# Performance work log

Hardware: AMD Instinct MI355X
Metric: run time of the kernel (lower is better)

Reference implementation:

```python
import jax, jax.numpy as jnp
import numpy as np

E = 8        # n_routed_experts
TOPK = 2     # num_experts_per_tok


def setup_inputs() -> dict:
    key = jax.random.key(0)
    k0, k1, k2, k3, k4 = jax.random.split(key, 5)
    B, S, D, H = 1, 2048, 1024, 2816
    scale = 0.02
    x = jax.random.normal(k0, (B, S, D), jnp.float32)
    Wg = jax.random.normal(k1, (E, D), jnp.float32) * scale   # gate weight [E, D]
    W1 = jax.random.normal(k2, (E, H, D), jnp.float32) * scale  # up-gate proj
    W2 = jax.random.normal(k3, (E, D, H), jnp.float32) * scale  # down proj
    W3 = jax.random.normal(k4, (E, H, D), jnp.float32) * scale  # up proj
    return {"x": x, "Wg": Wg, "W1": W1, "W2": W2, "W3": W3}


def _moe_forward(x, Wg, W1, W2, W3):
    B, S, D = x.shape
    xt = x.reshape(-1, D)                      # [T, D], T = B*S
    T = xt.shape[0]
    # --- gate: logits -> softmax -> top-k, normalized top-k weights ---
    logits = xt @ Wg.T                         # [T, E]
    scores = jax.nn.softmax(logits, axis=-1)
    w, idx = jax.lax.top_k(scores, TOPK)       # [T, K]
    w = w / (w.sum(axis=-1, keepdims=True) + 1e-20)
    # combine weights per token per expert (scatter top-k weights) [T, E]
    cw = jnp.zeros((T, E), xt.dtype).at[jnp.arange(T)[:, None], idx].add(w)
    # --- per-expert SwiGLU FFN (batched over experts) ---
    h = jax.nn.silu(jnp.einsum('td,ehd->teh', xt, W1)) * jnp.einsum('td,ehd->teh', xt, W3)  # [T,E,H]
    out = jnp.einsum('teh,edh->ted', h, W2)    # [T, E, D]
    # weighted combine of selected experts (cw is zero for unselected)
    y = jnp.einsum('te,ted->td', cw, out)      # [T, D]
    return y.reshape(B, S, D)


def reference(x, Wg, W1, W2, W3):
    return _moe_forward(x, Wg, W1, W2, W3)
```

## Files before the change

### kernel.cpp

```cpp
#include <hip/hip_runtime.h>
#include <hip/hip_bf16.h>

#define T_TOK 2048
#define D_DIM 1024
#define H_DIM 2816
#define E_NUM 8
#define CAP   1024

typedef __attribute__((ext_vector_type(8))) short short8;
typedef __attribute__((ext_vector_type(4))) float floatx4;

__device__ __forceinline__ unsigned short f2bf(float f) {
    unsigned int b = __float_as_uint(f);
    b += 0x7FFFu + ((b >> 16) & 1u);
    return (unsigned short)(b >> 16);
}

__device__ __forceinline__ unsigned pk2(float lo, float hi) {
    unsigned a = __float_as_uint(lo) + 0x8000u;
    unsigned b = __float_as_uint(hi) + 0x8000u;
    return __builtin_amdgcn_perm(b, a, 0x07060302);
}

__device__ __forceinline__ short8 pack8r(float4 a, float4 b) {
    union { uint4 u; short8 s; } r;
    r.u.x = pk2(a.x, a.y);
    r.u.y = pk2(a.z, a.w);
    r.u.z = pk2(b.x, b.y);
    r.u.w = pk2(b.z, b.w);
    return r.s;
}

__device__ __forceinline__ void gl2lds16(const void* g, void* l) {
    __builtin_amdgcn_global_load_lds(
        (const __attribute__((address_space(1))) unsigned int*)g,
        (__attribute__((address_space(3))) unsigned int*)l,
        16, 0, 0);
}


__global__ __launch_bounds__(256) void k_gate2(const float* __restrict__ x,
                                               const float* __restrict__ Wg,
                                               int* __restrict__ stok,
                                               float* __restrict__ sw,
                                               int* __restrict__ counts,
                                               unsigned short* __restrict__ xg) {
    const int wave = threadIdx.x >> 6, lane = threadIdx.x & 63;
    const int t = blockIdx.x * 4 + wave;
    const float* xr = x + (size_t)t * D_DIM;
    float acc[E_NUM];
#pragma unroll
    for (int e = 0; e < E_NUM; ++e) acc[e] = 0.f;
#pragma unroll 4
    for (int i = 0; i < D_DIM / 64; ++i) {
        float xv = xr[lane + 64 * i];
#pragma unroll
        for (int e = 0; e < E_NUM; ++e) acc[e] += xv * Wg[e * D_DIM + lane + 64 * i];
    }
#pragma unroll
    for (int e = 0; e < E_NUM; ++e) {
#pragma unroll
        for (int s = 32; s > 0; s >>= 1) acc[e] += __shfl_xor(acc[e], s, 64);
    }
    int slot0 = 0, slot1 = 0;
    if (lane == 0) {
        float mx = acc[0];
#pragma unroll
        for (int e = 1; e < E_NUM; ++e) mx = fmaxf(mx, acc[e]);
        float p[E_NUM], s = 0.f;
#pragma unroll
        for (int e = 0; e < E_NUM; ++e) { p[e] = __expf(acc[e] - mx); s += p[e]; }
        int i0 = 0;
#pragma unroll
        for (int e = 1; e < E_NUM; ++e) if (p[e] > p[i0]) i0 = e;
        int i1 = (i0 == 0) ? 1 : 0;
#pragma unroll
        for (int e = 0; e < E_NUM; ++e) if (e != i0 && p[e] > p[i1]) i1 = e;
        float s0 = p[i0] / s, s1 = p[i1] / s;
        float d = s0 + s1 + 1e-20f;
        int p0 = atomicAdd(&counts[i0], 1); if (p0 >= CAP) p0 = CAP - 1;
        int p1 = atomicAdd(&counts[i1], 1); if (p1 >= CAP) p1 = CAP - 1;
        slot0 = i0 * CAP + p0;
        slot1 = i1 * CAP + p1;
        stok[slot0] = t; sw[slot0] = s0 / d;
        stok[slot1] = t; sw[slot1] = s1 / d;
    }
    slot0 = __shfl(slot0, 0, 64);
    slot1 = __shfl(slot1, 0, 64);
    const float4* xr4 = (const float4*)xr;
    ushort4* xg4 = (ushort4*)xg;
#pragma unroll
    for (int it = 0; it < 4; ++it) {
        float4 v = xr4[lane + 64 * it];
        ushort4 o;
        o.x = f2bf(v.x); o.y = f2bf(v.y); o.z = f2bf(v.z); o.w = f2bf(v.w);
        xg4[(size_t)slot0 * 256 + lane + 64 * it] = o;
        xg4[(size_t)slot1 * 256 + lane + 64 * it] = o;
    }
}

__device__ __forceinline__ void g13_tile(const unsigned char* Ab, const unsigned char* B1b,
                                         const unsigned char* B3b, int agrp, int c0, int c1,
                                         int f8, int f7,
                                         floatx4 (&acc1)[4][2], floatx4 (&acc3)[4][2]) {
    short8 b1f[2][2], b3f[2][2];
#pragma unroll
    for (int n = 0; n < 2; ++n) {
        const int bg = (n * 2 + f8) * 1024 + f7 * 128;
        b1f[n][0] = *(const short8*)(B1b + bg + c0);
        b1f[n][1] = *(const short8*)(B1b + bg + c1);
        b3f[n][0] = *(const short8*)(B3b + bg + c0);
        b3f[n][1] = *(const short8*)(B3b + bg + c1);
    }
#pragma unroll
    for (int m = 0; m < 4; ++m) {
        const unsigned char* ab = Ab + agrp + m * 2048;
        short8 a0 = *(const short8*)(ab + c0);
        short8 a1 = *(const short8*)(ab + c1);
#pragma unroll
        for (int n = 0; n < 2; ++n) {
            acc1[m][n] = __builtin_amdgcn_mfma_f32_16x16x32_bf16(a0, b1f[n][0], acc1[m][n], 0, 0, 0);
            acc1[m][n] = __builtin_amdgcn_mfma_f32_16x16x32_bf16(a1, b1f[n][1], acc1[m][n], 0, 0, 0);
            acc3[m][n] = __builtin_amdgcn_mfma_f32_16x16x32_bf16(a0, b3f[n][0], acc3[m][n], 0, 0, 0);
            acc3[m][n] = __builtin_amdgcn_mfma_f32_16x16x32_bf16(a1, b3f[n][1], acc3[m][n], 0, 0, 0);
        }
    }
}

__global__ __launch_bounds__(256, 2) void k_gemm13(const unsigned short* __restrict__ xg,
                                                   const float* __restrict__ W1,
                                                   const float* __restrict__ W3,
                                                   const int* __restrict__ counts,
                                                   unsigned short* __restrict__ U) {
    const int nt = blockIdx.x;
    const int mt = blockIdx.y;
    const int e  = blockIdx.z;
    const int cnt = min(counts[e], CAP);
    if (mt * 256 >= cnt) return;

    __shared__ __align__(16) unsigned char As[2][32768];
    __shared__ __align__(16) unsigned char B1s[2][4096];
    __shared__ __align__(16) unsigned char B3s[2][4096];

    const int tid = threadIdx.x, lane = tid & 63, wave = tid >> 6;
    const int fr = lane & 15, quad = lane >> 4, f7 = fr & 7, f8 = fr >> 3;

    const unsigned short* aBase = xg
        + ((size_t)e * CAP + mt * 256 + wave * 64 + (lane >> 3)) * D_DIM
        + ((lane & 7) ^ (lane >> 3)) * 8;

    const int br = tid >> 3, bc = tid & 7;
    const float* w1p = W1 + ((size_t)e * H_DIM + nt * 32 + br) * D_DIM + bc * 8;
    const float* w3p = W3 + ((size_t)e * H_DIM + nt * 32 + br) * D_DIM + bc * 8;
    const int bslot = (br >> 3) * 1024 + (br & 7) * 128 + ((bc ^ (br & 7)) << 4);

    floatx4 acc1[4][2], acc3[4][2];
#pragma unroll
    for (int m = 0; m < 4; ++m)
#pragma unroll
        for (int n = 0; n < 2; ++n) { acc1[m][n] = (floatx4)0.f; acc3[m][n] = (floatx4)0.f; }

    const int agrp = (wave * 8 + f8) * 1024 + f7 * 128;
    const int c0 = (quad ^ f7) << 4;
    const int c1 = ((4 | quad) ^ f7) << 4;

#pragma unroll
    for (int j = 0; j < 8; ++j)
        gl2lds16(aBase + (size_t)j * 8 * D_DIM, As[0] + (wave * 8 + j) * 1024);
    {
        float4 u0 = *(const float4*)(w1p);
        float4 u1 = *(const float4*)(w1p + 4);
        float4 v0 = *(const float4*)(w3p);
        float4 v1 = *(const float4*)(w3p + 4);
        *(short8*)(B1s[0] + bslot) = pack8r(u0, u1);
        *(short8*)(B3s[0] + bslot) = pack8r(v0, v1);
    }
    __syncthreads();

    int cur = 0;
#pragma unroll 1
    for (int t = 0; t < D_DIM / 64 - 1; ++t) {
        const int kn = (t + 1) * 64;
#pragma unroll
        for (int j = 0; j < 8; ++j)
            gl2lds16(aBase + (size_t)j * 8 * D_DIM + kn, As[cur ^ 1] + (wave * 8 + j) * 1024);
        float4 u0 = *(const float4*)(w1p + kn);
        float4 u1 = *(const float4*)(w1p + kn + 4);
        float4 v0 = *(const float4*)(w3p + kn);
        float4 v1 = *(const float4*)(w3p + kn + 4);

        g13_tile(As[cur], B1s[cur], B3s[cur], agrp, c0, c1, f8, f7, acc1, acc3);

        *(short8*)(B1s[cur ^ 1] + bslot) = pack8r(u0, u1);
        *(short8*)(B3s[cur ^ 1] + bslot) = pack8r(v0, v1);
        __syncthreads();
        cur ^= 1;
    }
    g13_tile(As[cur], B1s[cur], B3s[cur], agrp, c0, c1, f8, f7, acc1, acc3);

#pragma unroll
    for (int m = 0; m < 4; ++m) {
#pragma unroll
        for (int r = 0; r < 4; ++r) {
            int g = mt * 256 + wave * 64 + m * 16 + quad * 4 + r;
            if (g < cnt) {
                size_t rowb = ((size_t)e * CAP + g) * H_DIM + nt * 32;
#pragma unroll
                for (int n = 0; n < 2; ++n) {
                    float u1v = acc1[m][n][r], u3v = acc3[m][n][r];
                    float u = u1v / (1.f + __expf(-u1v)) * u3v;
                    U[rowb + n * 16 + fr] = f2bf(u);
                }
            }
        }
    }
}

__device__ __forceinline__ void g2_tile(const unsigned char* Ab, const unsigned char* Bb,
                                        int agrp, int c0, int c1, int f8, int f7,
                                        floatx4 (&acc)[4][4]) {
    short8 bf[4][2];
#pragma unroll
    for (int n = 0; n < 4; ++n) {
        const int bg = (n * 2 + f8) * 1024 + f7 * 128;
        bf[n][0] = *(const short8*)(Bb + bg + c0);
        bf[n][1] = *(const short8*)(Bb + bg + c1);
    }
#pragma unroll
    for (int m = 0; m < 4; ++m) {
        const unsigned char* ab = Ab + agrp + m * 2048;
        short8 a0 = *(const short8*)(ab + c0);
        short8 a1 = *(const short8*)(ab + c1);
#pragma unroll
        for (int n = 0; n < 4; ++n) {
            acc[m][n] = __builtin_amdgcn_mfma_f32_16x16x32_bf16(a0, bf[n][0], acc[m][n], 0, 0, 0);
            acc[m][n] = __builtin_amdgcn_mfma_f32_16x16x32_bf16(a1, bf[n][1], acc[m][n], 0, 0, 0);
        }
    }
}

__global__ __launch_bounds__(256, 2) void k_gemm2(const unsigned short* __restrict__ U,
                                                  const float* __restrict__ W2,
                                                  const int* __restrict__ counts,
                                                  const int* __restrict__ stok,
                                                  const float* __restrict__ sw,
                                                  float* __restrict__ y) {
    const int nt = blockIdx.x;
    const int mt = blockIdx.y;
    const int e  = blockIdx.z;
    const int cnt = min(counts[e], CAP);
    if (mt * 256 >= cnt) return;

    __shared__ __align__(16) unsigned char As[2][32768];
    __shared__ __align__(16) unsigned char Bs[2][8192];

    const int tid = threadIdx.x, lane = tid & 63, wave = tid >> 6;
    const int fr = lane & 15, quad = lane >> 4, f7 = fr & 7, f8 = fr >> 3;

    const unsigned short* aBase = U
        + ((size_t)e * CAP + mt * 256 + wave * 64 + (lane >> 3)) * H_DIM
        + ((lane & 7) ^ (lane >> 3)) * 8;

    const int br = tid >> 3, bc = tid & 7;
    const float* w2p0 = W2 + ((size_t)e * D_DIM + nt * 64 + br) * H_DIM + bc * 8;
    const float* w2p1 = w2p0 + (size_t)32 * H_DIM;
    const int bslot0 = (br >> 3) * 1024 + (br & 7) * 128 + ((bc ^ (br & 7)) << 4);
    const int bslot1 = bslot0 + 4096;

    floatx4 acc[4][4];
#pragma unroll
    for (int m = 0; m < 4; ++m)
#pragma unroll
        for (int n = 0; n < 4; ++n) acc[m][n] = (floatx4)0.f;

    const int agrp = (wave * 8 + f8) * 1024 + f7 * 128;
    const int c0 = (quad ^ f7) << 4;
    const int c1 = ((4 | quad) ^ f7) << 4;

#pragma unroll
    for (int j = 0; j < 8; ++j)
        gl2lds16(aBase + (size_t)j * 8 * H_DIM, As[0] + (wave * 8 + j) * 1024);
    {
        float4 u0 = *(const float4*)(w2p0);
        float4 u1 = *(const float4*)(w2p0 + 4);
        float4 v0 = *(const float4*)(w2p1);
        float4 v1 = *(const float4*)(w2p1 + 4);
        *(short8*)(Bs[0] + bslot0) = pack8r(u0, u1);
        *(short8*)(Bs[0] + bslot1) = pack8r(v0, v1);
    }
    __syncthreads();

    int cur = 0;
#pragma unroll 1
    for (int t = 0; t < H_DIM / 64 - 1; ++t) {
        const int kn = (t + 1) * 64;
#pragma unroll
        for (int j = 0; j < 8; ++j)
            gl2lds16(aBase + (size_t)j * 8 * H_DIM + kn, As[cur ^ 1] + (wave * 8 + j) * 1024);
        float4 u0 = *(const float4*)(w2p0 + kn);
        float4 u1 = *(const float4*)(w2p0 + kn + 4);
        float4 v0 = *(const float4*)(w2p1 + kn);
        float4 v1 = *(const float4*)(w2p1 + kn + 4);

        g2_tile(As[cur], Bs[cur], agrp, c0, c1, f8, f7, acc);

        *(short8*)(Bs[cur ^ 1] + bslot0) = pack8r(u0, u1);
        *(short8*)(Bs[cur ^ 1] + bslot1) = pack8r(v0, v1);
        __syncthreads();
        cur ^= 1;
    }
    g2_tile(As[cur], Bs[cur], agrp, c0, c1, f8, f7, acc);

#pragma unroll
    for (int m = 0; m < 4; ++m) {
#pragma unroll
        for (int r = 0; r < 4; ++r) {
            int g = mt * 256 + wave * 64 + m * 16 + quad * 4 + r;
            if (g < cnt) {
                int slot = e * CAP + g;
                int t = stok[slot];
                float w = sw[slot];
                float* yr = y + (size_t)t * D_DIM + nt * 64;
#pragma unroll
                for (int n = 0; n < 4; ++n)
                    atomicAdd(&yr[n * 16 + fr], w * acc[m][n][r]);
            }
        }
    }
}

static const size_t OFF_XG   = 0;
static const size_t OFF_U    = (size_t)E_NUM * CAP * D_DIM * 2;
static const size_t OFF_STOK = OFF_U + (size_t)E_NUM * CAP * H_DIM * 2;
static const size_t OFF_SW   = OFF_STOK + (size_t)E_NUM * CAP * 4;
static const size_t OFF_META = OFF_SW + (size_t)E_NUM * CAP * 4;

extern "C" void kernel_launch(void* const* d_in, const int* in_sizes, int n_in,
                              void* d_out, int out_size, void* d_ws, size_t ws_size,
                              hipStream_t stream) {
    const float* x  = (const float*)d_in[0];
    const float* Wg = (const float*)d_in[1];
    const float* W1 = (const float*)d_in[2];
    const float* W2 = (const float*)d_in[3];
    const float* W3 = (const float*)d_in[4];
    float* y = (float*)d_out;
    char* ws = (char*)d_ws;

    unsigned short* xg = (unsigned short*)(ws + OFF_XG);
    unsigned short* U  = (unsigned short*)(ws + OFF_U);
    int*   stok   = (int*)(ws + OFF_STOK);
    float* sw     = (float*)(ws + OFF_SW);
    int*   counts = (int*)(ws + OFF_META);

    hipMemsetAsync(counts, 0, 64, stream);
    hipMemsetAsync(y, 0, (size_t)T_TOK * D_DIM * sizeof(float), stream);

    k_gate2<<<T_TOK / 4, 256, 0, stream>>>(x, Wg, stok, sw, counts, xg);
    k_gemm13<<<dim3(H_DIM / 32, CAP / 256, E_NUM), 256, 0, stream>>>(xg, W1, W3, counts, U);
    k_gemm2<<<dim3(D_DIM / 64, CAP / 256, E_NUM), 256, 0, stream>>>(U, W2, counts, stok, sw, y);
}
```

Baseline: 481.6 us.

## Single-buffer LDS with register prefetch of fragments before async tile loads

Both expert GEMM kernels drop LDS double-buffering. Each iteration now reads all A and B fragments into registers, syncs, then issues the next tile's global-to-LDS loads into the same buffer while running MFMAs from registers. This halves shared memory per block, which could allow more resident blocks, and keeps load/compute overlap. In exchange it adds a second barrier per iteration and more fragment registers, which may hurt occupancy or latency hiding.

```diff
diff --git a/kernel.cpp b/kernel.cpp
--- a/kernel.cpp
+++ b/kernel.cpp
@@ -99,34 +99,6 @@
     }
 }
 
-__device__ __forceinline__ void g13_tile(const unsigned char* Ab, const unsigned char* B1b,
-                                         const unsigned char* B3b, int agrp, int c0, int c1,
-                                         int f8, int f7,
-                                         floatx4 (&acc1)[4][2], floatx4 (&acc3)[4][2]) {
-    short8 b1f[2][2], b3f[2][2];
-#pragma unroll
-    for (int n = 0; n < 2; ++n) {
-        const int bg = (n * 2 + f8) * 1024 + f7 * 128;
-        b1f[n][0] = *(const short8*)(B1b + bg + c0);
-        b1f[n][1] = *(const short8*)(B1b + bg + c1);
-        b3f[n][0] = *(const short8*)(B3b + bg + c0);
-        b3f[n][1] = *(const short8*)(B3b + bg + c1);
-    }
-#pragma unroll
-    for (int m = 0; m < 4; ++m) {
-        const unsigned char* ab = Ab + agrp + m * 2048;
-        short8 a0 = *(const short8*)(ab + c0);
-        short8 a1 = *(const short8*)(ab + c1);
-#pragma unroll
-        for (int n = 0; n < 2; ++n) {
-            acc1[m][n] = __builtin_amdgcn_mfma_f32_16x16x32_bf16(a0, b1f[n][0], acc1[m][n], 0, 0, 0);
-            acc1[m][n] = __builtin_amdgcn_mfma_f32_16x16x32_bf16(a1, b1f[n][1], acc1[m][n], 0, 0, 0);
-            acc3[m][n] = __builtin_amdgcn_mfma_f32_16x16x32_bf16(a0, b3f[n][0], acc3[m][n], 0, 0, 0);
-            acc3[m][n] = __builtin_amdgcn_mfma_f32_16x16x32_bf16(a1, b3f[n][1], acc3[m][n], 0, 0, 0);
-        }
-    }
-}
-
 __global__ __launch_bounds__(256, 2) void k_gemm13(const unsigned short* __restrict__ xg,
                                                    const float* __restrict__ W1,
                                                    const float* __restrict__ W3,
@@ -138,9 +110,9 @@
     const int cnt = min(counts[e], CAP);
     if (mt * 256 >= cnt) return;
 
-    __shared__ __align__(16) unsigned char As[2][32768];
-    __shared__ __align__(16) unsigned char B1s[2][4096];
-    __shared__ __align__(16) unsigned char B3s[2][4096];
+    __shared__ __align__(16) unsigned char As[32768];
+    __shared__ __align__(16) unsigned char B1s[4096];
+    __shared__ __align__(16) unsigned char B3s[4096];
 
     const int tid = threadIdx.x, lane = tid & 63, wave = tid >> 6;
     const int fr = lane & 15, quad = lane >> 4, f7 = fr & 7, f8 = fr >> 3;
@@ -166,37 +138,66 @@
 
 #pragma unroll
     for (int j = 0; j < 8; ++j)
-        gl2lds16(aBase + (size_t)j * 8 * D_DIM, As[0] + (wave * 8 + j) * 1024);
+        gl2lds16(aBase + (size_t)j * 8 * D_DIM, As + (wave * 8 + j) * 1024);
     {
         float4 u0 = *(const float4*)(w1p);
         float4 u1 = *(const float4*)(w1p + 4);
         float4 v0 = *(const float4*)(w3p);
         float4 v1 = *(const float4*)(w3p + 4);
-        *(short8*)(B1s[0] + bslot) = pack8r(u0, u1);
-        *(short8*)(B3s[0] + bslot) = pack8r(v0, v1);
+        *(short8*)(B1s + bslot) = pack8r(u0, u1);
+        *(short8*)(B3s + bslot) = pack8r(v0, v1);
     }
     __syncthreads();
 
-    int cur = 0;
 #pragma unroll 1
-    for (int t = 0; t < D_DIM / 64 - 1; ++t) {
-        const int kn = (t + 1) * 64;
-#pragma unroll
-        for (int j = 0; j < 8; ++j)
-            gl2lds16(aBase + (size_t)j * 8 * D_DIM + kn, As[cur ^ 1] + (wave * 8 + j) * 1024);
-        float4 u0 = *(const float4*)(w1p + kn);
-        float4 u1 = *(const float4*)(w1p + kn + 4);
-        float4 v0 = *(const float4*)(w3p + kn);
-        float4 v1 = *(const float4*)(w3p + kn + 4);
-
-        g13_tile(As[cur], B1s[cur], B3s[cur], agrp, c0, c1, f8, f7, acc1, acc3);
-
-        *(short8*)(B1s[cur ^ 1] + bslot) = pack8r(u0, u1);
-        *(short8*)(B3s[cur ^ 1] + bslot) = pack8r(v0, v1);
+    for (int t = 0; t < D_DIM / 64; ++t) {
+        short8 a[4][2], b1[2][2], b3[2][2];
+#pragma unroll
+        for (int m = 0; m < 4; ++m) {
+            const unsigned char* ab = As + agrp + m * 2048;
+            a[m][0] = *(const short8*)(ab + c0);
+            a[m][1] = *(const short8*)(ab + c1);
+        }
+#pragma unroll
+        for (int n = 0; n < 2; ++n) {
+            const int bg = (n * 2 + f8) * 1024 + f7 * 128;
+            b1[n][0] = *(const short8*)(B1s + bg + c0);
+            b1[n][1] = *(const short8*)(B1s + bg + c1);
+            b3[n][0] = *(const short8*)(B3s + bg + c0);
+            b3[n][1] = *(const short8*)(B3s + bg + c1);
+        }
         __syncthreads();
-        cur ^= 1;
-    }
-    g13_tile(As[cur], B1s[cur], B3s[cur], agrp, c0, c1, f8, f7, acc1, acc3);
+
+        const bool more = (t < D_DIM / 64 - 1);
+        float4 u0, u1, v0, v1;
+        if (more) {
+            const int kn = (t + 1) * 64;
+#pragma unroll
+            for (int j = 0; j < 8; ++j)
+                gl2lds16(aBase + (size_t)j * 8 * D_DIM + kn, As + (wave * 8 + j) * 1024);
+            u0 = *(const float4*)(w1p + kn);
+            u1 = *(const float4*)(w1p + kn + 4);
+            v0 = *(const float4*)(w3p + kn);
+            v1 = *(const float4*)(w3p + kn + 4);
+        }
+
+#pragma unroll
+        for (int m = 0; m < 4; ++m) {
+#pragma unroll
+            for (int n = 0; n < 2; ++n) {
+                acc1[m][n] = __builtin_amdgcn_mfma_f32_16x16x32_bf16(a[m][0], b1[n][0], acc1[m][n], 0, 0, 0);
+                acc1[m][n] = __builtin_amdgcn_mfma_f32_16x16x32_bf16(a[m][1], b1[n][1], acc1[m][n], 0, 0, 0);
+                acc3[m][n] = __builtin_amdgcn_mfma_f32_16x16x32_bf16(a[m][0], b3[n][0], acc3[m][n], 0, 0, 0);
+                acc3[m][n] = __builtin_amdgcn_mfma_f32_16x16x32_bf16(a[m][1], b3[n][1], acc3[m][n], 0, 0, 0);
+            }
+        }
+
+        if (more) {
+            *(short8*)(B1s + bslot) = pack8r(u0, u1);
+            *(short8*)(B3s + bslot) = pack8r(v0, v1);
+            __syncthreads();
+        }
+    }
 
 #pragma unroll
     for (int m = 0; m < 4; ++m) {
@@ -212,29 +213,6 @@
                     U[rowb + n * 16 + fr] = f2bf(u);
                 }
             }
-        }
-    }
-}
-
-__device__ __forceinline__ void g2_tile(const unsigned char* Ab, const unsigned char* Bb,
-                                        int agrp, int c0, int c1, int f8, int f7,
-                                        floatx4 (&acc)[4][4]) {
-    short8 bf[4][2];
-#pragma unroll
-    for (int n = 0; n < 4; ++n) {
-        const int bg = (n * 2 + f8) * 1024 + f7 * 128;
-        bf[n][0] = *(const short8*)(Bb + bg + c0);
-        bf[n][1] = *(const short8*)(Bb + bg + c1);
-    }
-#pragma unroll
-    for (int m = 0; m < 4; ++m) {
-        const unsigned char* ab = Ab + agrp + m * 2048;
-        short8 a0 = *(const short8*)(ab + c0);
-        short8 a1 = *(const short8*)(ab + c1);
-#pragma unroll
-        for (int n = 0; n < 4; ++n) {
-            acc[m][n] = __builtin_amdgcn_mfma_f32_16x16x32_bf16(a0, bf[n][0], acc[m][n], 0, 0, 0);
-            acc[m][n] = __builtin_amdgcn_mfma_f32_16x16x32_bf16(a1, bf[n][1], acc[m][n], 0, 0, 0);
         }
     }
 }
@@ -251,8 +229,8 @@
     const int cnt = min(counts[e], CAP);
     if (mt * 256 >= cnt) return;
 
-    __shared__ __align__(16) unsigned char As[2][32768];
-    __shared__ __align__(16) unsigned char Bs[2][8192];
+    __shared__ __align__(16) unsigned char As[32768];
+    __shared__ __align__(16) unsigned char Bs[8192];
 
     const int tid = threadIdx.x, lane = tid & 63, wave = tid >> 6;
     const int fr = lane & 15, quad = lane >> 4, f7 = fr & 7, f8 = fr >> 3;
@@ -279,37 +257,62 @@
 
 #pragma unroll
     for (int j = 0; j < 8; ++j)
-        gl2lds16(aBase + (size_t)j * 8 * H_DIM, As[0] + (wave * 8 + j) * 1024);
+        gl2lds16(aBase + (size_t)j * 8 * H_DIM, As + (wave * 8 + j) * 1024);
     {
         float4 u0 = *(const float4*)(w2p0);
         float4 u1 = *(const float4*)(w2p0 + 4);
         float4 v0 = *(const float4*)(w2p1);
         float4 v1 = *(const float4*)(w2p1 + 4);
-        *(short8*)(Bs[0] + bslot0) = pack8r(u0, u1);
-        *(short8*)(Bs[0] + bslot1) = pack8r(v0, v1);
+        *(short8*)(Bs + bslot0) = pack8r(u0, u1);
+        *(short8*)(Bs + bslot1) = pack8r(v0, v1);
     }
     __syncthreads();
 
-    int cur = 0;
 #pragma unroll 1
-    for (int t = 0; t < H_DIM / 64 - 1; ++t) {
-        const int kn = (t + 1) * 64;
-#pragma unroll
-        for (int j = 0; j < 8; ++j)
-            gl2lds16(aBase + (size_t)j * 8 * H_DIM + kn, As[cur ^ 1] + (wave * 8 + j) * 1024);
-        float4 u0 = *(const float4*)(w2p0 + kn);
-        float4 u1 = *(const float4*)(w2p0 + kn + 4);
-        float4 v0 = *(const float4*)(w2p1 + kn);
-        float4 v1 = *(const float4*)(w2p1 + kn + 4);
-
-        g2_tile(As[cur], Bs[cur], agrp, c0, c1, f8, f7, acc);
-
-        *(short8*)(Bs[cur ^ 1] + bslot0) = pack8r(u0, u1);
-        *(short8*)(Bs[cur ^ 1] + bslot1) = pack8r(v0, v1);
+    for (int t = 0; t < H_DIM / 64; ++t) {
+        short8 a[4][2], bf[4][2];
+#pragma unroll
+        for (int m = 0; m < 4; ++m) {
+            const unsigned char* ab = As + agrp + m * 2048;
+            a[m][0] = *(const short8*)(ab + c0);
+            a[m][1] = *(const short8*)(ab + c1);
+        }
+#pragma unroll
+        for (int n = 0; n < 4; ++n) {
+            const int bg = (n * 2 + f8) * 1024 + f7 * 128;
+            bf[n][0] = *(const short8*)(Bs + bg + c0);
+            bf[n][1] = *(const short8*)(Bs + bg + c1);
+        }
         __syncthreads();
-        cur ^= 1;
-    }
-    g2_tile(As[cur], Bs[cur], agrp, c0, c1, f8, f7, acc);
+
+        const bool more = (t < H_DIM / 64 - 1);
+        float4 u0, u1, v0, v1;
+        if (more) {
+            const int kn = (t + 1) * 64;
+#pragma unroll
+            for (int j = 0; j < 8; ++j)
+                gl2lds16(aBase + (size_t)j * 8 * H_DIM + kn, As + (wave * 8 + j) * 1024);
+            u0 = *(const float4*)(w2p0 + kn);
+            u1 = *(const float4*)(w2p0 + kn + 4);
+            v0 = *(const float4*)(w2p1 + kn);
+            v1 = *(const float4*)(w2p1 + kn + 4);
+        }
+
+#pragma unroll
+        for (int m = 0; m < 4; ++m) {
+#pragma unroll
+            for (int n = 0; n < 4; ++n) {
+                acc[m][n] = __builtin_amdgcn_mfma_f32_16x16x32_bf16(a[m][0], bf[n][0], acc[m][n], 0, 0, 0);
+                acc[m][n] = __builtin_amdgcn_mfma_f32_16x16x32_bf16(a[m][1], bf[n][1], acc[m][n], 0, 0, 0);
+            }
+        }
+
+        if (more) {
+            *(short8*)(Bs + bslot0) = pack8r(u0, u1);
+            *(short8*)(Bs + bslot1) = pack8r(v0, v1);
+            __syncthreads();
+        }
+    }
 
 #pragma unroll
     for (int m = 0; m < 4; ++m) {
```

Measured after the change: 431.2 us. 1.12x faster.
